# Kernel optimization log

Hardware: AMD Instinct MI355X
Metric: run time of the kernel (lower is better)

## Reference

```python
import jax, jax.numpy as jnp
import numpy as np

D_MODEL = 1024
NHEADS = 16
E_HEAD = D_MODEL // NHEADS  # 64
ROPE_BASE = 10000.0


def _rope_cos_sin(L, dim, base, dtype):
    # dim = E_head (even); inv_freq over pairs, GPT-NeoX half-split convention
    inv_freq = 1.0 / (base ** (jnp.arange(0, dim, 2, dtype=jnp.float32) / dim))
    pos = jnp.arange(L, dtype=jnp.float32)
    freqs = pos[:, None] * inv_freq[None, :]  # [L, dim/2]
    return jnp.cos(freqs).astype(dtype), jnp.sin(freqs).astype(dtype)


def _apply_rope(t, cos, sin):
    # t: [B, H, L, Dh]; rotate-half formulation
    d2 = t.shape[-1] // 2
    t1, t2 = t[..., :d2], t[..., d2:]
    return jnp.concatenate([t1 * cos - t2 * sin, t1 * sin + t2 * cos], axis=-1)


def setup_inputs() -> dict:
    key = jax.random.key(0)
    ks = jax.random.split(key, 5)
    B, L = 4, 2048
    x = jax.random.normal(ks[0], (B, L, D_MODEL), dtype=jnp.float32)
    s_in = 1.0 / np.sqrt(D_MODEL)
    W_packed = jax.random.normal(ks[1], (3 * D_MODEL, D_MODEL), dtype=jnp.float32) * s_in
    b_packed = jax.random.normal(ks[2], (3 * D_MODEL,), dtype=jnp.float32) * 0.02
    W_out = jax.random.normal(ks[3], (D_MODEL, D_MODEL), dtype=jnp.float32) * s_in
    b_out = jax.random.normal(ks[4], (D_MODEL,), dtype=jnp.float32) * 0.02
    return {"x": x, "W_packed": W_packed, "b_packed": b_packed, "W_out": W_out, "b_out": b_out}


def reference(x, W_packed, b_packed, W_out, b_out):
    B, L, _ = x.shape
    # 1) packed QKV projection (query is key is value path)
    qkv = jnp.einsum('ble,fe->blf', x, W_packed) + b_packed  # [B, L, 3*D]
    q, k, v = jnp.split(qkv, 3, axis=-1)
    # 2) split heads -> [B, H, L, Dh]
    def heads(t):
        return t.reshape(B, L, NHEADS, E_HEAD).transpose(0, 2, 1, 3)
    q, k, v = heads(q), heads(k), heads(v)
    # 3) RoPE on q, k
    cos, sin = _rope_cos_sin(L, E_HEAD, ROPE_BASE, x.dtype)
    q = _apply_rope(q, cos, sin)
    k = _apply_rope(k, cos, sin)
    # 4) SDPA (non-causal, no dropout)
    scale = 1.0 / np.sqrt(E_HEAD)
    scores = jnp.einsum('bhqd,bhkd->bhqk', q, k) * scale
    attn = jax.nn.softmax(scores, axis=-1)
    out = jnp.einsum('bhqk,bhkd->bhqd', attn, v)
    # 5) merge heads + output projection
    out = out.transpose(0, 2, 1, 3).reshape(B, L, D_MODEL)
    return jnp.einsum('bld,ed->ble', out, W_out) + b_out
```

## Files before the change

### kernel.cpp

```cpp
#include <hip/hip_runtime.h>
#include <hip/hip_bf16.h>
#include <stdint.h>

#define L_SEQ 2048
#define NB    4
#define NH    16
#define EH    64
#define DM    1024
#define MTOT  (NB * L_SEQ)

typedef __attribute__((ext_vector_type(8))) short bf16x8;
typedef __attribute__((ext_vector_type(4))) float f32x4;
typedef __attribute__((ext_vector_type(16))) float f32x16;

static __device__ __forceinline__ float bf2f(short u) {
    union { unsigned int i; float f; } c;
    c.i = ((unsigned int)(unsigned short)u) << 16;
    return c.f;
}
static __device__ __forceinline__ short f2bf(float f) {
    union { float f; unsigned int i; } c; c.f = f;
    unsigned int x = c.i;
    unsigned int r = (x + 0x7fffu + ((x >> 16) & 1u)) >> 16;
    return (short)(unsigned short)r;
}
static __device__ __forceinline__ unsigned cvtpk(float lo, float hi) {
    unsigned r;
    asm volatile("v_cvt_pk_bf16_f32 %0, %1, %2" : "=v"(r) : "v"(lo), "v"(hi));
    return r;
}

static __device__ __forceinline__ void gload_lds16(const void* g, void* lds) {
    __builtin_amdgcn_global_load_lds(
        (const __attribute__((address_space(1))) unsigned int*)g,
        (__attribute__((address_space(3))) unsigned int*)lds, 16, 0, 0);
}

__global__ __launch_bounds__(256) void cvt3_k(const float* __restrict__ x,
                                              const float* __restrict__ wp,
                                              const float* __restrict__ wo,
                                              short* __restrict__ xb,
                                              short* __restrict__ wpb,
                                              short* __restrict__ wob,
                                              float* __restrict__ tab) {
    int bid = blockIdx.x;
    if (bid >= 12288) {
        int i = (bid - 12288) * 256 + threadIdx.x;
        int l = i >> 5, d = i & 31;
        float inv = powf(10000.0f, -(float)d * (1.0f / 32.0f));
        float fr = (float)l * inv;
        tab[i]         = cosf(fr);
        tab[65536 + i] = sinf(fr);
        return;
    }
    const float* src; short* dst; int i;
    if (bid < 8192)       { src = x;  dst = xb;  i = bid * 256 + threadIdx.x; }
    else if (bid < 11264) { src = wp; dst = wpb; i = (bid - 8192) * 256 + threadIdx.x; }
    else                  { src = wo; dst = wob; i = (bid - 11264) * 256 + threadIdx.x; }
    float4 v = ((const float4*)src)[i];
    short4 o;
    o.x = f2bf(v.x); o.y = f2bf(v.y); o.z = f2bf(v.z); o.w = f2bf(v.w);
    ((short4*)dst)[i] = o;
}

template<int OUTBF16, int NBN, int NCOL, int EPI>
__global__ __launch_bounds__(512, 2) void gemmA_k(const short* __restrict__ A,
                                                  const short* __restrict__ Bt,
                                                  const float* __restrict__ bias,
                                                  void* __restrict__ Cv,
                                                  short* __restrict__ Qp,
                                                  short* __restrict__ Kp,
                                                  short* __restrict__ Vt) {
    __shared__ short lds[3][384 * 32];
    const int t = threadIdx.x;
    const int w = t >> 6, l = t & 63;
    const int wm = w >> 1, wn = w & 1;
    const int lr = l & 15, lh = l >> 4;

    const int nblk = NBN * 32;
    int fid = blockIdx.x + blockIdx.y * NBN;
    int swz = (fid & 7) * (nblk >> 3) + (fid >> 3);
    const int n0 = (swz % NBN) * 128;
    const int m0 = (swz / NBN) * 256;

    const int lrow = l >> 2;
    const int schunk = (l & 3) ^ ((l >> 3) & 3);

    const short* Ag = A + (size_t)(m0 + lrow) * 1024 + schunk * 8;
    const short* Bg = Bt + (size_t)(n0 + lrow) * 1024 + schunk * 8;

    auto STAGE = [&](int kt, short* dst) {
        gload_lds16(Ag + (size_t)(w * 32) * 1024 + kt * 32,      dst + (w * 32) * 32);
        gload_lds16(Ag + (size_t)(w * 32 + 16) * 1024 + kt * 32, dst + (w * 32 + 16) * 32);
        gload_lds16(Bg + (size_t)(w * 16) * 1024 + kt * 32,      dst + 8192 + (w * 16) * 32);
    };

    f32x4 acc[4][4] = {};

    STAGE(0, &lds[0][0]);
    STAGE(1, &lds[1][0]);
    asm volatile("s_waitcnt vmcnt(3)" ::: "memory");
    __builtin_amdgcn_s_barrier();

    short* Pc = &lds[0][0];
    short* Pn = &lds[1][0];
    short* Pf = &lds[2][0];

    const int fch = (lh ^ ((lr >> 1) & 3)) << 3;

    for (int kt = 0; kt < 32; ++kt) {
        if (kt < 30) STAGE(kt + 2, Pf);

        const short* Al = Pc;
        const short* Bl = Pc + 8192;

        bf16x8 bfr[4], af[4];
#pragma unroll
        for (int nj = 0; nj < 4; ++nj)
            bfr[nj] = *(const bf16x8*)(Bl + (wn * 64 + nj * 16 + lr) * 32 + fch);
#pragma unroll
        for (int mi = 0; mi < 4; ++mi)
            af[mi] = *(const bf16x8*)(Al + (wm * 64 + mi * 16 + lr) * 32 + fch);

        __builtin_amdgcn_s_setprio(1);
#pragma unroll
        for (int mi = 0; mi < 4; ++mi)
#pragma unroll
            for (int nj = 0; nj < 4; ++nj)
                acc[mi][nj] = __builtin_amdgcn_mfma_f32_16x16x32_bf16(
                    af[mi], bfr[nj], acc[mi][nj], 0, 0, 0);
        __builtin_amdgcn_s_setprio(0);

        asm volatile("s_waitcnt lgkmcnt(0)" ::: "memory");
        if (kt < 30) asm volatile("s_waitcnt vmcnt(3)" ::: "memory");
        else         asm volatile("s_waitcnt vmcnt(0)" ::: "memory");
        __builtin_amdgcn_s_barrier();

        short* tp = Pc; Pc = Pn; Pn = Pf; Pf = tp;
    }

    if (EPI == 0) {
#pragma unroll
        for (int mi = 0; mi < 4; ++mi) {
#pragma unroll
            for (int nj = 0; nj < 4; ++nj) {
                const int row = m0 + wm * 64 + mi * 16 + lh * 4;
                const int col = n0 + wn * 64 + nj * 16 + lr;
                const float bsv = bias[col];
#pragma unroll
                for (int j = 0; j < 4; ++j) {
                    float v = acc[mi][nj][j] + bsv;
                    if (OUTBF16)
                        ((short*)Cv)[(size_t)(row + j) * NCOL + col] = f2bf(v);
                    else
                        ((float*)Cv)[(size_t)(row + j) * NCOL + col] = v;
                }
            }
        }
    } else {
        const int part = n0 >> 10;
        const int h = ((n0 & 1023) >> 6) + wn;
#pragma unroll
        for (int mi = 0; mi < 4; ++mi) {
            const int r0 = m0 + wm * 64 + mi * 16 + lh * 4;
            const int bq = r0 >> 11, lq = r0 & 2047;
            if (part < 2) {
                short* Drow = (part == 0 ? Qp : Kp) + ((size_t)(bq * 16 + h) * 2048 + lq) * 64;
#pragma unroll
                for (int nj = 0; nj < 4; ++nj) {
                    const int d = nj * 16 + lr;
                    const float bsv = bias[n0 + wn * 64 + d];
#pragma unroll
                    for (int j = 0; j < 4; ++j)
                        Drow[j * 64 + d] = f2bf(acc[mi][nj][j] + bsv);
                }
            } else {
                const int lpb = (lq & ~63) + (((mi * 2 + (lh & 1)) ^ (lr & 7)) << 3) + ((lh >> 1) * 4);
#pragma unroll
                for (int nj = 0; nj < 4; ++nj) {
                    const int d = nj * 16 + lr;
                    const float bsv = bias[n0 + wn * 64 + d];
                    short4 sv;
                    sv.x = f2bf(acc[mi][nj][0] + bsv);
                    sv.y = f2bf(acc[mi][nj][1] + bsv);
                    sv.z = f2bf(acc[mi][nj][2] + bsv);
                    sv.w = f2bf(acc[mi][nj][3] + bsv);
                    *(short4*)(Vt + (size_t)((bq * 16 + h) * 64 + d) * 2048 + lpb) = sv;
                }
            }
        }
    }
}

__global__ __launch_bounds__(256) void krope_k(const short* __restrict__ Kpre,
                                               const float* __restrict__ tab,
                                               short* __restrict__ Kd) {
    int idx = blockIdx.x * 256 + threadIdx.x;
    int dp = (idx & 7) * 4;
    int h = (idx >> 3) & 15;
    int bl = idx >> 7;
    int l = bl & (L_SEQ - 1);
    int b = bl >> 11;
    float4 cs = *(const float4*)&tab[l * 32 + dp];
    float4 sn = *(const float4*)&tab[65536 + l * 32 + dp];
    size_t ob = ((size_t)((b * 16 + h) * 2048 + l)) * 64;
    const short* src = Kpre + ob;
    short4 k1 = *(const short4*)&src[dp];
    short4 k2 = *(const short4*)&src[dp + 32];
    union { unsigned u[2]; short4 s4; } e1, e2;
    e1.u[0] = cvtpk(bf2f(k1.x) * cs.x - bf2f(k2.x) * sn.x,
                    bf2f(k1.y) * cs.y - bf2f(k2.y) * sn.y);
    e1.u[1] = cvtpk(bf2f(k1.z) * cs.z - bf2f(k2.z) * sn.z,
                    bf2f(k1.w) * cs.w - bf2f(k2.w) * sn.w);
    e2.u[0] = cvtpk(bf2f(k1.x) * sn.x + bf2f(k2.x) * cs.x,
                    bf2f(k1.y) * sn.y + bf2f(k2.y) * cs.y);
    e2.u[1] = cvtpk(bf2f(k1.z) * sn.z + bf2f(k2.z) * cs.z,
                    bf2f(k1.w) * sn.w + bf2f(k2.w) * cs.w);
    int r7 = l & 7;
    int c1 = ((dp >> 3) ^ r7) * 8 + (dp & 7);
    int c2 = (((dp >> 3) | 4) ^ r7) * 8 + (dp & 7);
    *(short4*)(Kd + ob + c1) = e1.s4;
    *(short4*)(Kd + ob + c2) = e2.s4;
}

__global__ __launch_bounds__(512, 2) void attn_k(const short* __restrict__ Qpre,
                                                 const short* __restrict__ Kg,
                                                 const short* __restrict__ Vt,
                                                 const float* __restrict__ tab,
                                                 short* __restrict__ O) {
    __shared__ short Ks[3][64 * 64];
    __shared__ short Vs[3][64 * 64];
    const int t = threadIdx.x;
    const int w = t >> 6, l = t & 63;
    const int q = l & 31, hi = l >> 5;
    const int r7 = l & 7;

    const int od = blockIdx.x + blockIdx.y * 8;
    const int qblk = (od >> 3) & 7;
    const int bh = (od & 7) * 8 + (od >> 6);
    const int q0 = qblk * 256;

    const short* Kb = Kg + (size_t)bh * (2048 * 64);
    const short* Vb = Vt + (size_t)bh * (64 * 2048);

    const int qrow = q0 + w * 32 + q;

    const short* Qsrc = Qpre + (size_t)bh * (2048 * 64) + (size_t)qrow * 64;
    bf16x8 qraw[4];
#pragma unroll
    for (int ds = 0; ds < 4; ds++)
        qraw[ds] = *(const bf16x8*)(Qsrc + ds * 16 + hi * 8);
    const float sc = 0.18033688011112042f;
    bf16x8 qf[4];
#pragma unroll
    for (int dsL = 0; dsL < 2; dsL++) {
        const float* tc = tab + qrow * 32 + dsL * 16 + hi * 8;
        float4 ca = *(const float4*)tc;
        float4 cb = *(const float4*)(tc + 4);
        float4 sa = *(const float4*)(tc + 65536);
        float4 sb = *(const float4*)(tc + 65536 + 4);
        const float cv[8] = {ca.x, ca.y, ca.z, ca.w, cb.x, cb.y, cb.z, cb.w};
        const float sv[8] = {sa.x, sa.y, sa.z, sa.w, sb.x, sb.y, sb.z, sb.w};
        union { unsigned u[4]; bf16x8 v; } lo, hg;
#pragma unroll
        for (int p = 0; p < 4; p++) {
            float a0 = bf2f(qraw[dsL][2 * p]),     b0 = bf2f(qraw[dsL + 2][2 * p]);
            float a1 = bf2f(qraw[dsL][2 * p + 1]), b1 = bf2f(qraw[dsL + 2][2 * p + 1]);
            lo.u[p] = cvtpk((a0 * cv[2 * p] - b0 * sv[2 * p]) * sc,
                            (a1 * cv[2 * p + 1] - b1 * sv[2 * p + 1]) * sc);
            hg.u[p] = cvtpk((a0 * sv[2 * p] + b0 * cv[2 * p]) * sc,
                            (a1 * sv[2 * p + 1] + b1 * cv[2 * p + 1]) * sc);
        }
        qf[dsL] = lo.v; qf[dsL + 2] = hg.v;
    }

    const short one_bf = (short)0x3F80;
    const bf16x8 ones = {one_bf, one_bf, one_bf, one_bf, one_bf, one_bf, one_bf, one_bf};

    f32x16 o0 = {}, o1 = {}, os = {};

    const int grow = w * 8 + (l >> 3);
    const int gcol = r7 * 8;

    gload_lds16(Kb + (size_t)grow * 64 + gcol,        &Ks[0][w * 512]);
    gload_lds16(Vb + (size_t)grow * 2048 + gcol,      &Vs[0][w * 512]);
    gload_lds16(Kb + (size_t)(64 + grow) * 64 + gcol, &Ks[1][w * 512]);
    gload_lds16(Vb + (size_t)grow * 2048 + 64 + gcol, &Vs[1][w * 512]);
    asm volatile("s_waitcnt vmcnt(2)" ::: "memory");
    __builtin_amdgcn_s_barrier();

    const short* Kc = &Ks[0][0];  const short* Vc = &Vs[0][0];
    const short* Kn = &Ks[1][0];  const short* Vn = &Vs[1][0];
    short*       Kf = &Ks[2][0];  short*       Vf = &Vs[2][0];

    for (int it = 0; it < 32; ++it) {
        if (it < 30) {
            const int kn = (it + 2) * 64;
            gload_lds16(Kb + (size_t)(kn + grow) * 64 + gcol, Kf + w * 512);
            gload_lds16(Vb + (size_t)grow * 2048 + kn + gcol, Vf + w * 512);
        }

        f32x16 s0 = {}, s1 = {};
#pragma unroll
        for (int ds = 0; ds < 4; ds++) {
            const int ch = ((ds << 1) | hi) ^ r7;
            bf16x8 k0f = *(const bf16x8*)(Kc + q * 64 + ch * 8);
            bf16x8 k1f = *(const bf16x8*)(Kc + (32 + q) * 64 + ch * 8);
            __builtin_amdgcn_s_setprio(1);
            s0 = __builtin_amdgcn_mfma_f32_32x32x16_bf16(k0f, qf[ds], s0, 0, 0, 0);
            s1 = __builtin_amdgcn_mfma_f32_32x32x16_bf16(k1f, qf[ds], s1, 0, 0, 0);
            __builtin_amdgcn_s_setprio(0);
        }

#pragma unroll
        for (int r = 0; r < 16; r++) {
            s0[r] = __builtin_amdgcn_exp2f(s0[r]);
            s1[r] = __builtin_amdgcn_exp2f(s1[r]);
        }

        bf16x8 pf[4];
        {
            union { unsigned u[4]; bf16x8 v; } f;
            f.u[0] = cvtpk(s0[0], s0[1]);  f.u[1] = cvtpk(s0[2], s0[3]);
            f.u[2] = cvtpk(s0[4], s0[5]);  f.u[3] = cvtpk(s0[6], s0[7]);
            pf[0] = f.v;
            f.u[0] = cvtpk(s0[8], s0[9]);  f.u[1] = cvtpk(s0[10], s0[11]);
            f.u[2] = cvtpk(s0[12], s0[13]); f.u[3] = cvtpk(s0[14], s0[15]);
            pf[1] = f.v;
            f.u[0] = cvtpk(s1[0], s1[1]);  f.u[1] = cvtpk(s1[2], s1[3]);
            f.u[2] = cvtpk(s1[4], s1[5]);  f.u[3] = cvtpk(s1[6], s1[7]);
            pf[2] = f.v;
            f.u[0] = cvtpk(s1[8], s1[9]);  f.u[1] = cvtpk(s1[10], s1[11]);
            f.u[2] = cvtpk(s1[12], s1[13]); f.u[3] = cvtpk(s1[14], s1[15]);
            pf[3] = f.v;
        }

#pragma unroll
        for (int ks = 0; ks < 4; ks++) {
            const int ch = ((ks << 1) | hi) ^ r7;
            bf16x8 v0f = *(const bf16x8*)(Vc + q * 64 + ch * 8);
            bf16x8 v1f = *(const bf16x8*)(Vc + (32 + q) * 64 + ch * 8);
            __builtin_amdgcn_s_setprio(1);
            o0 = __builtin_amdgcn_mfma_f32_32x32x16_bf16(v0f, pf[ks], o0, 0, 0, 0);
            o1 = __builtin_amdgcn_mfma_f32_32x32x16_bf16(v1f, pf[ks], o1, 0, 0, 0);
            os = __builtin_amdgcn_mfma_f32_32x32x16_bf16(ones, pf[ks], os, 0, 0, 0);
            __builtin_amdgcn_s_setprio(0);
        }

        asm volatile("s_waitcnt lgkmcnt(0)" ::: "memory");
        if (it < 30) asm volatile("s_waitcnt vmcnt(2)" ::: "memory");
        else         asm volatile("s_waitcnt vmcnt(0)" ::: "memory");
        __builtin_amdgcn_s_barrier();

        const short* tk = Kc; Kc = Kn; Kn = Kf; Kf = (short*)tk;
        const short* tv = Vc; Vc = Vn; Vn = Vf; Vf = (short*)tv;
    }

    const float inv = 1.0f / os[0];
    const int b = bh >> 4, h = bh & 15;
    short* Orow = O + (size_t)(b * 2048 + qrow) * 1024 + h * 64;
#pragma unroll
    for (int g = 0; g < 4; g++) {
        unsigned w0 = cvtpk(o0[g * 4 + 0] * inv, o0[g * 4 + 1] * inv);
        unsigned w1 = cvtpk(o0[g * 4 + 2] * inv, o0[g * 4 + 3] * inv);
        unsigned long long p0 = (unsigned long long)w0 | ((unsigned long long)w1 << 32);
        *(unsigned long long*)(Orow + g * 8 + hi * 4) = p0;
        unsigned w2 = cvtpk(o1[g * 4 + 0] * inv, o1[g * 4 + 1] * inv);
        unsigned w3 = cvtpk(o1[g * 4 + 2] * inv, o1[g * 4 + 3] * inv);
        unsigned long long p1 = (unsigned long long)w2 | ((unsigned long long)w3 << 32);
        *(unsigned long long*)(Orow + 32 + g * 8 + hi * 4) = p1;
    }
}

extern "C" void kernel_launch(void* const* d_in, const int* in_sizes, int n_in,
                              void* d_out, int out_size, void* d_ws, size_t ws_size,
                              hipStream_t stream) {
    const float* x  = (const float*)d_in[0];
    const float* Wp = (const float*)d_in[1];
    const float* bp = (const float*)d_in[2];
    const float* Wo = (const float*)d_in[3];
    const float* bo = (const float*)d_in[4];

    char* ws = (char*)d_ws;
    const size_t SZ_XB  = (size_t)MTOT * DM * 2;
    const size_t SZ_WPB = (size_t)3 * DM * DM * 2;
    const size_t SZ_WOB = (size_t)DM * DM * 2;
    const size_t SZ_BHLE = (size_t)MTOT * DM * 2;

    short* xb   = (short*)(ws);
    short* wpb  = (short*)(ws + SZ_XB);
    short* wob  = (short*)(ws + SZ_XB + SZ_WPB);
    short* Qpre = (short*)(ws + SZ_XB + SZ_WPB + SZ_WOB);
    short* Kpre = (short*)(ws + SZ_XB + SZ_WPB + SZ_WOB + SZ_BHLE);
    short* Kb   = (short*)(ws + SZ_XB + SZ_WPB + SZ_WOB + 2 * SZ_BHLE);
    short* Vtb  = (short*)(ws + SZ_XB + SZ_WPB + SZ_WOB + 3 * SZ_BHLE);
    short* Ob   = (short*)(ws + SZ_XB + SZ_WPB + SZ_WOB + 4 * SZ_BHLE);
    float* tab  = (float*)(ws + SZ_XB + SZ_WPB + SZ_WOB + 5 * SZ_BHLE);

    cvt3_k<<<12544, 256, 0, stream>>>(x, Wp, Wo, xb, wpb, wob, tab);

    gemmA_k<1, 24, 3072, 1><<<dim3(24, 32), 512, 0, stream>>>(
        xb, wpb, bp, nullptr, Qpre, Kpre, Vtb);

    krope_k<<<4096, 256, 0, stream>>>(Kpre, tab, Kb);

    attn_k<<<dim3(8, 64), 512, 0, stream>>>(Qpre, Kb, Vtb, tab, Ob);

    gemmA_k<0, 8, 1024, 0><<<dim3(8, 32), 512, 0, stream>>>(
        Ob, wob, bo, (float*)d_out, nullptr, nullptr, nullptr);
}
```

Baseline: 183.1 us.

## Process two 32-row query tiles per wave in attention to reuse K/V fragments

Each wave now handles 64 query rows (two 32-row tiles A and B) instead of 32, so each block covers 512 queries and the grid shrinks to 256 blocks. K and V fragments read from LDS are shared by twice as many MFMAs, halving K/V global and LDS traffic per query. The Q RoPE prologue is moved after the initial K/V prefetch issue so it overlaps those loads. This raises register pressure (more accumulators) and halves the number of blocks, which may lower occupancy or leave CUs idle on a 256-CU device.

```diff
diff --git a/kernel.cpp b/kernel.cpp
--- a/kernel.cpp
+++ b/kernel.cpp
@@ -235,49 +235,14 @@
     const int q = l & 31, hi = l >> 5;
     const int r7 = l & 7;
 
-    const int od = blockIdx.x + blockIdx.y * 8;
-    const int qblk = (od >> 3) & 7;
-    const int bh = (od & 7) * 8 + (od >> 6);
-    const int q0 = qblk * 256;
+    const int od = blockIdx.x + blockIdx.y * 4;
+    const int xcd = od & 7, jj = od >> 3;
+    const int qblk = jj & 3;
+    const int bh = xcd * 8 + (jj >> 2);
+    const int q0 = qblk * 512;
 
     const short* Kb = Kg + (size_t)bh * (2048 * 64);
     const short* Vb = Vt + (size_t)bh * (64 * 2048);
-
-    const int qrow = q0 + w * 32 + q;
-
-    const short* Qsrc = Qpre + (size_t)bh * (2048 * 64) + (size_t)qrow * 64;
-    bf16x8 qraw[4];
-#pragma unroll
-    for (int ds = 0; ds < 4; ds++)
-        qraw[ds] = *(const bf16x8*)(Qsrc + ds * 16 + hi * 8);
-    const float sc = 0.18033688011112042f;
-    bf16x8 qf[4];
-#pragma unroll
-    for (int dsL = 0; dsL < 2; dsL++) {
-        const float* tc = tab + qrow * 32 + dsL * 16 + hi * 8;
-        float4 ca = *(const float4*)tc;
-        float4 cb = *(const float4*)(tc + 4);
-        float4 sa = *(const float4*)(tc + 65536);
-        float4 sb = *(const float4*)(tc + 65536 + 4);
-        const float cv[8] = {ca.x, ca.y, ca.z, ca.w, cb.x, cb.y, cb.z, cb.w};
-        const float sv[8] = {sa.x, sa.y, sa.z, sa.w, sb.x, sb.y, sb.z, sb.w};
-        union { unsigned u[4]; bf16x8 v; } lo, hg;
-#pragma unroll
-        for (int p = 0; p < 4; p++) {
-            float a0 = bf2f(qraw[dsL][2 * p]),     b0 = bf2f(qraw[dsL + 2][2 * p]);
-            float a1 = bf2f(qraw[dsL][2 * p + 1]), b1 = bf2f(qraw[dsL + 2][2 * p + 1]);
-            lo.u[p] = cvtpk((a0 * cv[2 * p] - b0 * sv[2 * p]) * sc,
-                            (a1 * cv[2 * p + 1] - b1 * sv[2 * p + 1]) * sc);
-            hg.u[p] = cvtpk((a0 * sv[2 * p] + b0 * cv[2 * p]) * sc,
-                            (a1 * sv[2 * p + 1] + b1 * cv[2 * p + 1]) * sc);
-        }
-        qf[dsL] = lo.v; qf[dsL + 2] = hg.v;
-    }
-
-    const short one_bf = (short)0x3F80;
-    const bf16x8 ones = {one_bf, one_bf, one_bf, one_bf, one_bf, one_bf, one_bf, one_bf};
-
-    f32x16 o0 = {}, o1 = {}, os = {};
 
     const int grow = w * 8 + (l >> 3);
     const int gcol = r7 * 8;
@@ -286,7 +251,49 @@
     gload_lds16(Vb + (size_t)grow * 2048 + gcol,      &Vs[0][w * 512]);
     gload_lds16(Kb + (size_t)(64 + grow) * 64 + gcol, &Ks[1][w * 512]);
     gload_lds16(Vb + (size_t)grow * 2048 + 64 + gcol, &Vs[1][w * 512]);
-    asm volatile("s_waitcnt vmcnt(2)" ::: "memory");
+
+    const int qrowA = q0 + w * 64 + q;
+    const int qrowB = qrowA + 32;
+    const float sc = 0.18033688011112042f;
+
+    bf16x8 qfA[4], qfB[4];
+    auto ropeQ = [&](int qrow, bf16x8* qf) {
+        const short* Qsrc = Qpre + (size_t)bh * (2048 * 64) + (size_t)qrow * 64;
+        bf16x8 qraw[4];
+#pragma unroll
+        for (int ds = 0; ds < 4; ds++)
+            qraw[ds] = *(const bf16x8*)(Qsrc + ds * 16 + hi * 8);
+#pragma unroll
+        for (int dsL = 0; dsL < 2; dsL++) {
+            const float* tc = tab + qrow * 32 + dsL * 16 + hi * 8;
+            float4 ca = *(const float4*)tc;
+            float4 cb = *(const float4*)(tc + 4);
+            float4 sa = *(const float4*)(tc + 65536);
+            float4 sb = *(const float4*)(tc + 65536 + 4);
+            const float cv[8] = {ca.x, ca.y, ca.z, ca.w, cb.x, cb.y, cb.z, cb.w};
+            const float sv[8] = {sa.x, sa.y, sa.z, sa.w, sb.x, sb.y, sb.z, sb.w};
+            union { unsigned u[4]; bf16x8 v; } lo, hg;
+#pragma unroll
+            for (int p = 0; p < 4; p++) {
+                float a0 = bf2f(qraw[dsL][2 * p]),     b0 = bf2f(qraw[dsL + 2][2 * p]);
+                float a1 = bf2f(qraw[dsL][2 * p + 1]), b1 = bf2f(qraw[dsL + 2][2 * p + 1]);
+                lo.u[p] = cvtpk((a0 * cv[2 * p] - b0 * sv[2 * p]) * sc,
+                                (a1 * cv[2 * p + 1] - b1 * sv[2 * p + 1]) * sc);
+                hg.u[p] = cvtpk((a0 * sv[2 * p] + b0 * cv[2 * p]) * sc,
+                                (a1 * sv[2 * p + 1] + b1 * cv[2 * p + 1]) * sc);
+            }
+            qf[dsL] = lo.v; qf[dsL + 2] = hg.v;
+        }
+    };
+    ropeQ(qrowA, qfA);
+    ropeQ(qrowB, qfB);
+
+    const short one_bf = (short)0x3F80;
+    const bf16x8 ones = {one_bf, one_bf, one_bf, one_bf, one_bf, one_bf, one_bf, one_bf};
+
+    f32x16 oA0 = {}, oA1 = {}, oB0 = {}, oB1 = {}, osA = {}, osB = {};
+
+    asm volatile("s_waitcnt vmcnt(0)" ::: "memory");
     __builtin_amdgcn_s_barrier();
 
     const short* Kc = &Ks[0][0];  const short* Vc = &Vs[0][0];
@@ -300,39 +307,55 @@
             gload_lds16(Vb + (size_t)grow * 2048 + kn + gcol, Vf + w * 512);
         }
 
-        f32x16 s0 = {}, s1 = {};
+        f32x16 sA0 = {}, sA1 = {}, sB0 = {}, sB1 = {};
 #pragma unroll
         for (int ds = 0; ds < 4; ds++) {
             const int ch = ((ds << 1) | hi) ^ r7;
             bf16x8 k0f = *(const bf16x8*)(Kc + q * 64 + ch * 8);
             bf16x8 k1f = *(const bf16x8*)(Kc + (32 + q) * 64 + ch * 8);
             __builtin_amdgcn_s_setprio(1);
-            s0 = __builtin_amdgcn_mfma_f32_32x32x16_bf16(k0f, qf[ds], s0, 0, 0, 0);
-            s1 = __builtin_amdgcn_mfma_f32_32x32x16_bf16(k1f, qf[ds], s1, 0, 0, 0);
+            sA0 = __builtin_amdgcn_mfma_f32_32x32x16_bf16(k0f, qfA[ds], sA0, 0, 0, 0);
+            sA1 = __builtin_amdgcn_mfma_f32_32x32x16_bf16(k1f, qfA[ds], sA1, 0, 0, 0);
+            sB0 = __builtin_amdgcn_mfma_f32_32x32x16_bf16(k0f, qfB[ds], sB0, 0, 0, 0);
+            sB1 = __builtin_amdgcn_mfma_f32_32x32x16_bf16(k1f, qfB[ds], sB1, 0, 0, 0);
             __builtin_amdgcn_s_setprio(0);
         }
 
 #pragma unroll
         for (int r = 0; r < 16; r++) {
-            s0[r] = __builtin_amdgcn_exp2f(s0[r]);
-            s1[r] = __builtin_amdgcn_exp2f(s1[r]);
-        }
-
-        bf16x8 pf[4];
+            sA0[r] = __builtin_amdgcn_exp2f(sA0[r]);
+            sA1[r] = __builtin_amdgcn_exp2f(sA1[r]);
+            sB0[r] = __builtin_amdgcn_exp2f(sB0[r]);
+            sB1[r] = __builtin_amdgcn_exp2f(sB1[r]);
+        }
+
+        bf16x8 pfA[4], pfB[4];
         {
             union { unsigned u[4]; bf16x8 v; } f;
-            f.u[0] = cvtpk(s0[0], s0[1]);  f.u[1] = cvtpk(s0[2], s0[3]);
-            f.u[2] = cvtpk(s0[4], s0[5]);  f.u[3] = cvtpk(s0[6], s0[7]);
-            pf[0] = f.v;
-            f.u[0] = cvtpk(s0[8], s0[9]);  f.u[1] = cvtpk(s0[10], s0[11]);
-            f.u[2] = cvtpk(s0[12], s0[13]); f.u[3] = cvtpk(s0[14], s0[15]);
-            pf[1] = f.v;
-            f.u[0] = cvtpk(s1[0], s1[1]);  f.u[1] = cvtpk(s1[2], s1[3]);
-            f.u[2] = cvtpk(s1[4], s1[5]);  f.u[3] = cvtpk(s1[6], s1[7]);
-            pf[2] = f.v;
-            f.u[0] = cvtpk(s1[8], s1[9]);  f.u[1] = cvtpk(s1[10], s1[11]);
-            f.u[2] = cvtpk(s1[12], s1[13]); f.u[3] = cvtpk(s1[14], s1[15]);
-            pf[3] = f.v;
+            f.u[0] = cvtpk(sA0[0], sA0[1]);   f.u[1] = cvtpk(sA0[2], sA0[3]);
+            f.u[2] = cvtpk(sA0[4], sA0[5]);   f.u[3] = cvtpk(sA0[6], sA0[7]);
+            pfA[0] = f.v;
+            f.u[0] = cvtpk(sA0[8], sA0[9]);   f.u[1] = cvtpk(sA0[10], sA0[11]);
+            f.u[2] = cvtpk(sA0[12], sA0[13]); f.u[3] = cvtpk(sA0[14], sA0[15]);
+            pfA[1] = f.v;
+            f.u[0] = cvtpk(sA1[0], sA1[1]);   f.u[1] = cvtpk(sA1[2], sA1[3]);
+            f.u[2] = cvtpk(sA1[4], sA1[5]);   f.u[3] = cvtpk(sA1[6], sA1[7]);
+            pfA[2] = f.v;
+            f.u[0] = cvtpk(sA1[8], sA1[9]);   f.u[1] = cvtpk(sA1[10], sA1[11]);
+            f.u[2] = cvtpk(sA1[12], sA1[13]); f.u[3] = cvtpk(sA1[14], sA1[15]);
+            pfA[3] = f.v;
+            f.u[0] = cvtpk(sB0[0], sB0[1]);   f.u[1] = cvtpk(sB0[2], sB0[3]);
+            f.u[2] = cvtpk(sB0[4], sB0[5]);   f.u[3] = cvtpk(sB0[6], sB0[7]);
+            pfB[0] = f.v;
+            f.u[0] = cvtpk(sB0[8], sB0[9]);   f.u[1] = cvtpk(sB0[10], sB0[11]);
+            f.u[2] = cvtpk(sB0[12], sB0[13]); f.u[3] = cvtpk(sB0[14], sB0[15]);
+            pfB[1] = f.v;
+            f.u[0] = cvtpk(sB1[0], sB1[1]);   f.u[1] = cvtpk(sB1[2], sB1[3]);
+            f.u[2] = cvtpk(sB1[4], sB1[5]);   f.u[3] = cvtpk(sB1[6], sB1[7]);
+            pfB[2] = f.v;
+            f.u[0] = cvtpk(sB1[8], sB1[9]);   f.u[1] = cvtpk(sB1[10], sB1[11]);
+            f.u[2] = cvtpk(sB1[12], sB1[13]); f.u[3] = cvtpk(sB1[14], sB1[15]);
+            pfB[3] = f.v;
         }
 
 #pragma unroll
@@ -341,9 +364,12 @@
             bf16x8 v0f = *(const bf16x8*)(Vc + q * 64 + ch * 8);
             bf16x8 v1f = *(const bf16x8*)(Vc + (32 + q) * 64 + ch * 8);
             __builtin_amdgcn_s_setprio(1);
-            o0 = __builtin_amdgcn_mfma_f32_32x32x16_bf16(v0f, pf[ks], o0, 0, 0, 0);
-            o1 = __builtin_amdgcn_mfma_f32_32x32x16_bf16(v1f, pf[ks], o1, 0, 0, 0);
-            os = __builtin_amdgcn_mfma_f32_32x32x16_bf16(ones, pf[ks], os, 0, 0, 0);
+            oA0 = __builtin_amdgcn_mfma_f32_32x32x16_bf16(v0f, pfA[ks], oA0, 0, 0, 0);
+            oA1 = __builtin_amdgcn_mfma_f32_32x32x16_bf16(v1f, pfA[ks], oA1, 0, 0, 0);
+            oB0 = __builtin_amdgcn_mfma_f32_32x32x16_bf16(v0f, pfB[ks], oB0, 0, 0, 0);
+            oB1 = __builtin_amdgcn_mfma_f32_32x32x16_bf16(v1f, pfB[ks], oB1, 0, 0, 0);
+            osA = __builtin_amdgcn_mfma_f32_32x32x16_bf16(ones, pfA[ks], osA, 0, 0, 0);
+            osB = __builtin_amdgcn_mfma_f32_32x32x16_bf16(ones, pfB[ks], osB, 0, 0, 0);
             __builtin_amdgcn_s_setprio(0);
         }
 
@@ -356,19 +382,36 @@
         const short* tv = Vc; Vc = Vn; Vn = Vf; Vf = (short*)tv;
     }
 
-    const float inv = 1.0f / os[0];
     const int b = bh >> 4, h = bh & 15;
-    short* Orow = O + (size_t)(b * 2048 + qrow) * 1024 + h * 64;
-#pragma unroll
-    for (int g = 0; g < 4; g++) {
-        unsigned w0 = cvtpk(o0[g * 4 + 0] * inv, o0[g * 4 + 1] * inv);
-        unsigned w1 = cvtpk(o0[g * 4 + 2] * inv, o0[g * 4 + 3] * inv);
-        unsigned long long p0 = (unsigned long long)w0 | ((unsigned long long)w1 << 32);
-        *(unsigned long long*)(Orow + g * 8 + hi * 4) = p0;
-        unsigned w2 = cvtpk(o1[g * 4 + 0] * inv, o1[g * 4 + 1] * inv);
-        unsigned w3 = cvtpk(o1[g * 4 + 2] * inv, o1[g * 4 + 3] * inv);
-        unsigned long long p1 = (unsigned long long)w2 | ((unsigned long long)w3 << 32);
-        *(unsigned long long*)(Orow + 32 + g * 8 + hi * 4) = p1;
+    {
+        const float inv = 1.0f / osA[0];
+        short* Orow = O + (size_t)(b * 2048 + qrowA) * 1024 + h * 64;
+#pragma unroll
+        for (int g = 0; g < 4; g++) {
+            unsigned w0 = cvtpk(oA0[g * 4 + 0] * inv, oA0[g * 4 + 1] * inv);
+            unsigned w1 = cvtpk(oA0[g * 4 + 2] * inv, oA0[g * 4 + 3] * inv);
+            unsigned long long p0 = (unsigned long long)w0 | ((unsigned long long)w1 << 32);
+            *(unsigned long long*)(Orow + g * 8 + hi * 4) = p0;
+            unsigned w2 = cvtpk(oA1[g * 4 + 0] * inv, oA1[g * 4 + 1] * inv);
+            unsigned w3 = cvtpk(oA1[g * 4 + 2] * inv, oA1[g * 4 + 3] * inv);
+            unsigned long long p1 = (unsigned long long)w2 | ((unsigned long long)w3 << 32);
+            *(unsigned long long*)(Orow + 32 + g * 8 + hi * 4) = p1;
+        }
+    }
+    {
+        const float inv = 1.0f / osB[0];
+        short* Orow = O + (size_t)(b * 2048 + qrowB) * 1024 + h * 64;
+#pragma unroll
+        for (int g = 0; g < 4; g++) {
+            unsigned w0 = cvtpk(oB0[g * 4 + 0] * inv, oB0[g * 4 + 1] * inv);
+            unsigned w1 = cvtpk(oB0[g * 4 + 2] * inv, oB0[g * 4 + 3] * inv);
+            unsigned long long p0 = (unsigned long long)w0 | ((unsigned long long)w1 << 32);
+            *(unsigned long long*)(Orow + g * 8 + hi * 4) = p0;
+            unsigned w2 = cvtpk(oB1[g * 4 + 0] * inv, oB1[g * 4 + 1] * inv);
+            unsigned w3 = cvtpk(oB1[g * 4 + 2] * inv, oB1[g * 4 + 3] * inv);
+            unsigned long long p1 = (unsigned long long)w2 | ((unsigned long long)w3 << 32);
+            *(unsigned long long*)(Orow + 32 + g * 8 + hi * 4) = p1;
+        }
     }
 }
 
@@ -404,7 +447,7 @@
 
     krope_k<<<4096, 256, 0, stream>>>(Kpre, tab, Kb);
 
-    attn_k<<<dim3(8, 64), 512, 0, stream>>>(Qpre, Kb, Vtb, tab, Ob);
+    attn_k<<<dim3(4, 64), 512, 0, stream>>>(Qpre, Kb, Vtb, tab, Ob);
 
     gemmA_k<0, 8, 1024, 0><<<dim3(8, 32), 512, 0, stream>>>(
         Ob, wob, bo, (float*)d_out, nullptr, nullptr, nullptr);
```

Result: no change. 182.2 us (-0.5%).
